# Kernel optimization log

Measured on AMD Instinct MI355X. Metric: run time of the kernel, lower is better.

Reference implementation:

```python
import jax, jax.numpy as jnp
import numpy as np

B, T, H, W, D = 2, 8, 32, 32, 256
NUM_HEADS, KWIN_K = 8, 3
LN_EPS = 1e-5


def build_neighbor_idx(h, w, k):
    # Matches _build_indices: for each of N=h*w positions, the k*k clamped
    # (replicate-padded) neighbor flat indices. Returned as [N, k*k]
    # (already permuted like `idx.permute(1, 0)` in the torch forward).
    r = k // 2
    hh, ww = np.meshgrid(np.arange(h), np.arange(w), indexing='ij')
    nbrs = []
    for dh in range(-r, r + 1):
        for dw in range(-r, r + 1):
            nh = np.clip(hh + dh, 0, h - 1)
            nw = np.clip(ww + dw, 0, w - 1)
            nbrs.append((nh * w + nw).reshape(-1))
    return jnp.asarray(np.stack(nbrs, axis=1), dtype=jnp.int32)  # [N, k*k]


def setup_inputs() -> dict:
    key = jax.random.key(0)
    ks = jax.random.split(key, 9)
    s = 1.0 / np.sqrt(D)
    return {
        'x': jax.random.normal(ks[0], (B, T, H, W, D), dtype=jnp.float32),
        'ln_g': jnp.ones((D,), jnp.float32),
        'ln_b': jnp.zeros((D,), jnp.float32),
        'wq': jax.random.normal(ks[1], (D, D), jnp.float32) * s,
        'bq': jax.random.normal(ks[2], (D,), jnp.float32) * 0.01,
        'wk': jax.random.normal(ks[3], (D, D), jnp.float32) * s,
        'bk': jax.random.normal(ks[4], (D,), jnp.float32) * 0.01,
        'wv': jax.random.normal(ks[5], (D, D), jnp.float32) * s,
        'bv': jax.random.normal(ks[6], (D,), jnp.float32) * 0.01,
        'wo': jax.random.normal(ks[7], (D, D), jnp.float32) * s,
        'bo': jax.random.normal(ks[8], (D,), jnp.float32) * 0.01,
    }


def reference(x, ln_g, ln_b, wq, bq, wk, bk, wv, bv, wo, bo):
    # Dropout layers are identity (inference mode).
    b, t, h, w, d = x.shape
    n = h * w
    hd = d // NUM_HEADS
    x_ = x.reshape(b * t, n, d)

    # LayerNorm over last dim
    mu = jnp.mean(x_, axis=-1, keepdims=True)
    var = jnp.var(x_, axis=-1, keepdims=True)
    xn = (x_ - mu) * jax.lax.rsqrt(var + LN_EPS) * ln_g + ln_b

    q = xn @ wq + bq
    k_ = xn @ wk + bk
    v = xn @ wv + bv

    def split_heads(tns):  # [BT, N, D] -> [BT, heads, N, hd]
        return tns.reshape(b * t, n, NUM_HEADS, hd).transpose(0, 2, 1, 3)

    qh, kh, vh = split_heads(q), split_heads(k_), split_heads(v)

    idx = build_neighbor_idx(h, w, KWIN_K)  # [N, Kwin]
    # Gather neighbors directly (no expand): [BT, heads, N, Kwin, hd]
    k_local = kh[:, :, idx, :]
    v_local = vh[:, :, idx, :]

    scores = jnp.einsum('bhnd,bhnkd->bhnk', qh, k_local) / np.sqrt(hd)
    attn = jax.nn.softmax(scores, axis=-1)
    out = jnp.einsum('bhnk,bhnkd->bhnd', attn, v_local)

    out = out.transpose(0, 2, 1, 3).reshape(b * t, n, d)
    out = out @ wo + bo
    out = out + x_
    return out.reshape(b, t, h, w, d)
```

## Files before the change

kernel.cpp:

```cpp
#include <hip/hip_runtime.h>
#include <hip/hip_bf16.h>

#define M_TOT 16384
#define D_    256
#define K_DIM 256

typedef __attribute__((ext_vector_type(4))) float f32x4;
typedef __attribute__((ext_vector_type(8))) short s16x8;
typedef __attribute__((ext_vector_type(4))) short s16x4;

typedef const __attribute__((address_space(1))) void* gptr_t;
typedef __attribute__((address_space(3))) void* lptr_t;

__device__ __forceinline__ unsigned short f2bf(float f) {
  unsigned x = __float_as_uint(f);
  return (unsigned short)((x + 0x7fffu + ((x >> 16) & 1u)) >> 16);
}
__device__ __forceinline__ float bf2f(short s) {
  return __uint_as_float(((unsigned)(unsigned short)s) << 16);
}

__global__ __launch_bounds__(256) void prep_kernel(
    const float* __restrict__ x, const float* __restrict__ g, const float* __restrict__ b,
    unsigned short* __restrict__ xn,
    const float* __restrict__ wq, const float* __restrict__ wk,
    const float* __restrict__ wv, const float* __restrict__ wo,
    unsigned short* __restrict__ wt_qkv, unsigned short* __restrict__ wt_o) {
  __shared__ float tile[32][33];
  int tid = threadIdx.x;
  if (blockIdx.x < 4096) {
    int tok  = blockIdx.x * 4 + (tid >> 6);
    int lane = tid & 63;
    f32x4 v = ((const f32x4*)(x + (size_t)tok * D_))[lane];
    float s = 0.f, s2 = 0.f;
#pragma unroll
    for (int i = 0; i < 4; ++i) { s += v[i]; s2 += v[i] * v[i]; }
#pragma unroll
    for (int o = 1; o < 64; o <<= 1) { s += __shfl_xor(s, o); s2 += __shfl_xor(s2, o); }
    float mu   = s * (1.0f / 256.0f);
    float rstd = rsqrtf(s2 * (1.0f / 256.0f) - mu * mu + 1e-5f);
    f32x4 gv = ((const f32x4*)g)[lane];
    f32x4 bv = ((const f32x4*)b)[lane];
    s16x4 o4;
#pragma unroll
    for (int i = 0; i < 4; ++i) o4[i] = (short)f2bf((v[i] - mu) * rstd * gv[i] + bv[i]);
    ((s16x4*)(xn + (size_t)tok * D_))[lane] = o4;
  } else {
    int bid = blockIdx.x - 4096;
    int z   = bid >> 6;
    int rem = bid & 63;
    int k0 = (rem & 7) * 32, n0 = (rem >> 3) * 32;
    int tx = tid & 31, ty = tid >> 5;
    const float* src = (z == 0) ? wq : (z == 1) ? wk : (z == 2) ? wv : wo;
#pragma unroll
    for (int i = 0; i < 4; ++i) {
      int r = ty + i * 8;
      tile[r][tx] = src[(size_t)(k0 + r) * D_ + n0 + tx];
    }
    __syncthreads();
    unsigned short* dst = (z < 3) ? (wt_qkv + (size_t)(z * 256 + n0) * K_DIM + k0)
                                  : (wt_o + (size_t)n0 * K_DIM + k0);
#pragma unroll
    for (int i = 0; i < 4; ++i) {
      int r = ty + i * 8;
      dst[(size_t)r * K_DIM + tx] = f2bf(tile[tx][r]);
    }
  }
}

__global__ __launch_bounds__(256) void gemm_qkv_kernel(
    const unsigned short* __restrict__ A, const unsigned short* __restrict__ Bt,
    const float* __restrict__ b0, const float* __restrict__ b1, const float* __restrict__ b2,
    unsigned short* __restrict__ C) {
  __shared__ __align__(16) char smem[32768];
  char* Asm = smem;
  char* Bsm = smem + 16384;
  const int tid  = threadIdx.x;
  const int wid  = tid >> 6;
  const int lane = tid & 63;
  int lin = blockIdx.y * 6 + blockIdx.x;
  int swz = (lin & 7) * 96 + (lin >> 3);
  const int m0 = (swz / 6) * 128;
  const int n0 = (swz % 6) * 128;
  const int wave_m = wid >> 1;
  const int wave_n = wid & 1;

  f32x4 acc[4][4] = {};

  for (int ks = 0; ks < 4; ++ks) {
    const int kk0 = ks * 64;
    __syncthreads();
#pragma unroll
    for (int it = 0; it < 4; ++it) {
      int base     = (it * 256 + wid * 64) * 16;
      int lane_lin = base + lane * 16;
      int row  = lane_lin >> 7;
      int off  = lane_lin & 127;
      int soff = off ^ ((row & 7) << 4);
      const char* ga = (const char*)(A + (size_t)(m0 + row) * K_DIM + kk0) + soff;
      const char* gb = (const char*)(Bt + (size_t)(n0 + row) * K_DIM + kk0) + soff;
      __builtin_amdgcn_global_load_lds((gptr_t)ga, (lptr_t)(Asm + base), 16, 0, 0);
      __builtin_amdgcn_global_load_lds((gptr_t)gb, (lptr_t)(Bsm + base), 16, 0, 0);
    }
    __syncthreads();

#pragma unroll
    for (int kk = 0; kk < 2; ++kk) {
      s16x8 af[4], bf[4];
#pragma unroll
      for (int m = 0; m < 4; ++m) {
        int r    = wave_m * 64 + m * 16 + (lane & 15);
        int byte = kk * 64 + ((lane >> 4) * 16);
        af[m] = *(const s16x8*)(Asm + r * 128 + (byte ^ ((r & 7) << 4)));
      }
#pragma unroll
      for (int n = 0; n < 4; ++n) {
        int r    = wave_n * 64 + n * 16 + (lane & 15);
        int byte = kk * 64 + ((lane >> 4) * 16);
        bf[n] = *(const s16x8*)(Bsm + r * 128 + (byte ^ ((r & 7) << 4)));
      }
#pragma unroll
      for (int m = 0; m < 4; ++m)
#pragma unroll
        for (int n = 0; n < 4; ++n)
          acc[m][n] = __builtin_amdgcn_mfma_f32_16x16x32_bf16(af[m], bf[n], acc[m][n], 0, 0, 0);
    }
  }

  const int c0 = lane & 15;
  const int r0 = (lane >> 4) * 4;
#pragma unroll
  for (int m = 0; m < 4; ++m) {
#pragma unroll
    for (int n = 0; n < 4; ++n) {
      int row = m0 + wave_m * 64 + m * 16 + r0;
      int col = n0 + wave_n * 64 + n * 16 + c0;
      const float* bias = (col < 256) ? b0 : (col < 512) ? b1 : b2;
      float bb = bias[col & 255];
#pragma unroll
      for (int r = 0; r < 4; ++r)
        C[(size_t)(row + r) * 768 + col] = f2bf(acc[m][n][r] + bb);
    }
  }
}

__global__ __launch_bounds__(512, 4) void attn_ogemm_kernel(
    const unsigned short* __restrict__ qkv, const unsigned short* __restrict__ wto,
    const float* __restrict__ bo, const float* __restrict__ x,
    float* __restrict__ out) {
  __shared__ __align__(16) char smem[65536];
  char* Halo = smem;
  char* Asm  = smem + 49152;
  const int tid  = threadIdx.x;
  const int wid  = tid >> 6;
  const int lane = tid & 63;
  int bswz = (blockIdx.x & 7) * 64 + (blockIdx.x >> 3);
  const int bt = bswz >> 5;
  const int h  = bswz & 31;
  const int t0 = bswz * 32;
  const size_t img = (size_t)bt << 10;

  int srow[3];
  srow[0] = max(h - 1, 0); srow[1] = h; srow[2] = min(h + 1, 31);

#pragma unroll
  for (int sweep = 0; sweep < 6; ++sweep) {
    int chunk = sweep * 8 + wid;
    int slot = chunk >> 4, t2 = chunk & 15;
    int tokw = t2 * 2 + (lane >> 5);
    int off  = (lane & 31) * 16;
    size_t grow = img + (size_t)srow[slot] * 32 + tokw;
    const char* ga = (const char*)qkv + grow * 1536 + 512 + off;
    __builtin_amdgcn_global_load_lds((gptr_t)ga, (lptr_t)(Halo + chunk * 1024), 16, 0, 0);
  }
  s16x4 qr4[4];
#pragma unroll
  for (int i = 0; i < 4; ++i)
    qr4[i] = *(const s16x4*)(qkv + (size_t)(t0 + wid * 4 + i) * 768 + lane * 4);
  s16x4 vreg[3][6];
#pragma unroll
  for (int s = 0; s < 3; ++s) {
#pragma unroll
    for (int cr = 0; cr < 6; ++cr) {
      int cc = min(max(wid * 4 - 1 + cr, 0), 31);
      vreg[s][cr] = *(const s16x4*)(qkv + (img + (size_t)srow[s] * 32 + cc) * 768 +
                                    512 + lane * 4);
    }
  }
  __syncthreads();

#pragma unroll
  for (int i = 0; i < 4; ++i) {
    int tloc = wid * 4 + i;
    f32x4 q;
#pragma unroll
    for (int e = 0; e < 4; ++e) q[e] = bf2f(qr4[i][e]);
    float sc[9];
#pragma unroll
    for (int s = 0; s < 3; ++s) {
#pragma unroll
      for (int dw = -1; dw <= 1; ++dw) {
        const int j = s * 3 + (dw + 1);
        int cw = min(max(tloc + dw, 0), 31);
        s16x4 kr = *(const s16x4*)(Halo + (s * 32 + cw) * 512 + lane * 8);
        float p = 0.f;
#pragma unroll
        for (int e = 0; e < 4; ++e) p += q[e] * bf2f(kr[e]);
        p += __shfl_xor(p, 1);
        p += __shfl_xor(p, 2);
        p += __shfl_xor(p, 4);
        sc[j] = p * 0.17677669529663687f;
      }
    }
    float mx = sc[0];
#pragma unroll
    for (int j = 1; j < 9; ++j) mx = fmaxf(mx, sc[j]);
    float den = 0.f;
#pragma unroll
    for (int j = 0; j < 9; ++j) { sc[j] = __expf(sc[j] - mx); den += sc[j]; }
    float inv = 1.0f / den;
    f32x4 o = {};
#pragma unroll
    for (int s = 0; s < 3; ++s) {
#pragma unroll
      for (int dw = -1; dw <= 1; ++dw) {
        const int j = s * 3 + (dw + 1);
        float wj = sc[j] * inv;
        s16x4 vr = vreg[s][i + dw + 1];
#pragma unroll
        for (int e = 0; e < 4; ++e) o[e] += wj * bf2f(vr[e]);
      }
    }
    s16x4 ov;
#pragma unroll
    for (int e = 0; e < 4; ++e) ov[e] = (short)f2bf(o[e]);
    int byte = (lane * 8) ^ ((tloc & 7) << 4);
    *(s16x4*)(Asm + tloc * 512 + byte) = ov;
  }

  const int wave_m = wid >> 2;
  const int wave_n = wid & 3;
  f32x4 acc[4] = {};

  for (int ks = 0; ks < 4; ++ks) {
    __syncthreads();
#pragma unroll
    for (int it = 0; it < 4; ++it) {
      int base     = it * 8192 + wid * 1024;
      int lane_lin = base + lane * 16;
      int row  = lane_lin >> 7;
      int off  = lane_lin & 127;
      int soff = off ^ ((row & 7) << 4);
      const char* gb = (const char*)(wto + (size_t)row * K_DIM + ks * 64) + soff;
      __builtin_amdgcn_global_load_lds((gptr_t)gb, (lptr_t)(Halo + base), 16, 0, 0);
    }
    __syncthreads();

#pragma unroll
    for (int kk = 0; kk < 2; ++kk) {
      s16x8 af, bf[4];
      {
        int r    = wave_m * 16 + (lane & 15);
        int byte = ks * 128 + kk * 64 + ((lane >> 4) * 16);
        af = *(const s16x8*)(Asm + r * 512 + (byte ^ ((r & 7) << 4)));
      }
#pragma unroll
      for (int n = 0; n < 4; ++n) {
        int r    = wave_n * 64 + n * 16 + (lane & 15);
        int byte = kk * 64 + ((lane >> 4) * 16);
        bf[n] = *(const s16x8*)(Halo + r * 128 + (byte ^ ((r & 7) << 4)));
      }
#pragma unroll
      for (int n = 0; n < 4; ++n)
        acc[n] = __builtin_amdgcn_mfma_f32_16x16x32_bf16(af, bf[n], acc[n], 0, 0, 0);
    }
  }

  const int c0 = lane & 15;
  const int r0 = (lane >> 4) * 4;
#pragma unroll
  for (int n = 0; n < 4; ++n) {
    int col = wave_n * 64 + n * 16 + c0;
    float bb = bo[col];
#pragma unroll
    for (int r = 0; r < 4; ++r) {
      int row = t0 + wave_m * 16 + r0 + r;
      out[(size_t)row * D_ + col] = acc[n][r] + bb + x[(size_t)row * D_ + col];
    }
  }
}

extern "C" void kernel_launch(void* const* d_in, const int* in_sizes, int n_in,
                              void* d_out, int out_size, void* d_ws, size_t ws_size,
                              hipStream_t stream) {
  const float* x  = (const float*)d_in[0];
  const float* lg = (const float*)d_in[1];
  const float* lb = (const float*)d_in[2];
  const float* wq = (const float*)d_in[3];
  const float* bq = (const float*)d_in[4];
  const float* wk = (const float*)d_in[5];
  const float* bk = (const float*)d_in[6];
  const float* wv = (const float*)d_in[7];
  const float* bv = (const float*)d_in[8];
  const float* wo = (const float*)d_in[9];
  const float* bo = (const float*)d_in[10];
  float* out = (float*)d_out;

  char* ws = (char*)d_ws;
  unsigned short* xn    = (unsigned short*)ws;
  unsigned short* qkv   = (unsigned short*)(ws + 8388608);
  unsigned short* wtqkv = (unsigned short*)(ws + 33554432);
  unsigned short* wto   = (unsigned short*)(ws + 33947648);

  prep_kernel<<<4352, 256, 0, stream>>>(x, lg, lb, xn, wq, wk, wv, wo, wtqkv, wto);
  gemm_qkv_kernel<<<dim3(6, 128), 256, 0, stream>>>(xn, wtqkv, bq, bk, bv, qkv);
  attn_ogemm_kernel<<<512, 512, 0, stream>>>(qkv, wto, bo, x, out);
}
```

Baseline: 41.20 us.

## Load K neighbors into registers and prefetch first Wo tile during attention

K neighbor vectors are now read directly from global memory into registers instead of being staged as a halo in LDS. This shrinks shared memory from 64KB to 48KB, which may allow more resident blocks. The first Wo k-slice is issued to LDS before the attention computation so its latency overlaps that work, and the later slices load after each MFMA step. The cost is more register pressure from holding kreg alongside vreg, and duplicated K loads across waves instead of shared LDS reads.

```diff
diff --git a/kernel.cpp b/kernel.cpp
--- a/kernel.cpp
+++ b/kernel.cpp
@@ -148,9 +148,9 @@
     const unsigned short* __restrict__ qkv, const unsigned short* __restrict__ wto,
     const float* __restrict__ bo, const float* __restrict__ x,
     float* __restrict__ out) {
-  __shared__ __align__(16) char smem[65536];
-  char* Halo = smem;
-  char* Asm  = smem + 49152;
+  __shared__ __align__(16) char smem[49152];
+  char* Asm = smem;
+  char* Bsm = smem + 16384;
   const int tid  = threadIdx.x;
   const int wid  = tid >> 6;
   const int lane = tid & 63;
@@ -164,34 +164,34 @@
   srow[0] = max(h - 1, 0); srow[1] = h; srow[2] = min(h + 1, 31);
 
 #pragma unroll
-  for (int sweep = 0; sweep < 6; ++sweep) {
-    int chunk = sweep * 8 + wid;
-    int slot = chunk >> 4, t2 = chunk & 15;
-    int tokw = t2 * 2 + (lane >> 5);
-    int off  = (lane & 31) * 16;
-    size_t grow = img + (size_t)srow[slot] * 32 + tokw;
-    const char* ga = (const char*)qkv + grow * 1536 + 512 + off;
-    __builtin_amdgcn_global_load_lds((gptr_t)ga, (lptr_t)(Halo + chunk * 1024), 16, 0, 0);
-  }
+  for (int it = 0; it < 4; ++it) {
+    int base     = it * 8192 + wid * 1024;
+    int lane_lin = base + lane * 16;
+    int row  = lane_lin >> 7;
+    int off  = lane_lin & 127;
+    int soff = off ^ ((row & 7) << 4);
+    const char* gb = (const char*)(wto + (size_t)row * K_DIM + 0) + soff;
+    __builtin_amdgcn_global_load_lds((gptr_t)gb, (lptr_t)(Bsm + base), 16, 0, 0);
+  }
+
   s16x4 qr4[4];
 #pragma unroll
   for (int i = 0; i < 4; ++i)
     qr4[i] = *(const s16x4*)(qkv + (size_t)(t0 + wid * 4 + i) * 768 + lane * 4);
-  s16x4 vreg[3][6];
+  s16x4 kreg[3][6], vreg[3][6];
 #pragma unroll
   for (int s = 0; s < 3; ++s) {
 #pragma unroll
     for (int cr = 0; cr < 6; ++cr) {
       int cc = min(max(wid * 4 - 1 + cr, 0), 31);
-      vreg[s][cr] = *(const s16x4*)(qkv + (img + (size_t)srow[s] * 32 + cc) * 768 +
-                                    512 + lane * 4);
-    }
-  }
-  __syncthreads();
+      const unsigned short* rowp = qkv + (img + (size_t)srow[s] * 32 + cc) * 768;
+      kreg[s][cr] = *(const s16x4*)(rowp + 256 + lane * 4);
+      vreg[s][cr] = *(const s16x4*)(rowp + 512 + lane * 4);
+    }
+  }
 
 #pragma unroll
   for (int i = 0; i < 4; ++i) {
-    int tloc = wid * 4 + i;
     f32x4 q;
 #pragma unroll
     for (int e = 0; e < 4; ++e) q[e] = bf2f(qr4[i][e]);
@@ -201,8 +201,7 @@
 #pragma unroll
       for (int dw = -1; dw <= 1; ++dw) {
         const int j = s * 3 + (dw + 1);
-        int cw = min(max(tloc + dw, 0), 31);
-        s16x4 kr = *(const s16x4*)(Halo + (s * 32 + cw) * 512 + lane * 8);
+        s16x4 kr = kreg[s][i + dw + 1];
         float p = 0.f;
 #pragma unroll
         for (int e = 0; e < 4; ++e) p += q[e] * bf2f(kr[e]);
@@ -231,31 +230,20 @@
         for (int e = 0; e < 4; ++e) o[e] += wj * bf2f(vr[e]);
       }
     }
+    int tloc = wid * 4 + i;
     s16x4 ov;
 #pragma unroll
     for (int e = 0; e < 4; ++e) ov[e] = (short)f2bf(o[e]);
     int byte = (lane * 8) ^ ((tloc & 7) << 4);
     *(s16x4*)(Asm + tloc * 512 + byte) = ov;
   }
+  __syncthreads();
 
   const int wave_m = wid >> 2;
   const int wave_n = wid & 3;
   f32x4 acc[4] = {};
 
   for (int ks = 0; ks < 4; ++ks) {
-    __syncthreads();
-#pragma unroll
-    for (int it = 0; it < 4; ++it) {
-      int base     = it * 8192 + wid * 1024;
-      int lane_lin = base + lane * 16;
-      int row  = lane_lin >> 7;
-      int off  = lane_lin & 127;
-      int soff = off ^ ((row & 7) << 4);
-      const char* gb = (const char*)(wto + (size_t)row * K_DIM + ks * 64) + soff;
-      __builtin_amdgcn_global_load_lds((gptr_t)gb, (lptr_t)(Halo + base), 16, 0, 0);
-    }
-    __syncthreads();
-
 #pragma unroll
     for (int kk = 0; kk < 2; ++kk) {
       s16x8 af, bf[4];
@@ -268,11 +256,25 @@
       for (int n = 0; n < 4; ++n) {
         int r    = wave_n * 64 + n * 16 + (lane & 15);
         int byte = kk * 64 + ((lane >> 4) * 16);
-        bf[n] = *(const s16x8*)(Halo + r * 128 + (byte ^ ((r & 7) << 4)));
+        bf[n] = *(const s16x8*)(Bsm + r * 128 + (byte ^ ((r & 7) << 4)));
       }
 #pragma unroll
       for (int n = 0; n < 4; ++n)
         acc[n] = __builtin_amdgcn_mfma_f32_16x16x32_bf16(af, bf[n], acc[n], 0, 0, 0);
+    }
+    if (ks < 3) {
+      __syncthreads();
+#pragma unroll
+      for (int it = 0; it < 4; ++it) {
+        int base     = it * 8192 + wid * 1024;
+        int lane_lin = base + lane * 16;
+        int row  = lane_lin >> 7;
+        int off  = lane_lin & 127;
+        int soff = off ^ ((row & 7) << 4);
+        const char* gb = (const char*)(wto + (size_t)row * K_DIM + (ks + 1) * 64) + soff;
+        __builtin_amdgcn_global_load_lds((gptr_t)gb, (lptr_t)(Bsm + base), 16, 0, 0);
+      }
+      __syncthreads();
     }
   }
 
```

Result: faster. 39.60 us, median of 2 (-3.9%).
